# Performance work log

Hardware: AMD Instinct MI355X
Metric: run time of the kernel (lower is better)

## Reference

```python
import jax, jax.numpy as jnp
import numpy as np

INPUT_DIM = 2048
NUM_EXPERTS = 64
TOP_K = 2


def setup_inputs() -> dict:
    key = jax.random.key(0)
    kx, kw = jax.random.split(key)
    x = jax.random.normal(kx, (4, 4096, INPUT_DIM), dtype=jnp.float32)
    # nn.Linear weight has shape [num_experts, input_dim]
    W = jax.random.normal(kw, (NUM_EXPERTS, INPUT_DIM), dtype=jnp.float32) * (INPUT_DIM ** -0.5)
    return {"x": x, "W": W}


def reference(x, W):
    # Flatten tokens: [N, D]
    x_flat = x.reshape(-1, INPUT_DIM)
    # Gate logits: [N, E]
    gate_logits = jnp.einsum("nd,ed->ne", x_flat, W)
    # Top-k (sorted descending, matching torch.topk)
    top_k_logits, top_k_indices = jax.lax.top_k(gate_logits, TOP_K)
    top_k_values = jax.nn.softmax(top_k_logits, axis=-1)
    return (top_k_indices, top_k_values)
```

## Files before the change

kernel.cpp:

```cpp
#include <hip/hip_runtime.h>
#include <math.h>

typedef float f4 __attribute__((ext_vector_type(4)));
typedef float f32x4 __attribute__((ext_vector_type(4)));
typedef short bf16x8 __attribute__((ext_vector_type(8)));

#define D      2048
#define NE     64
#define TOKB   32
#define KSPLIT 4
#define KRNG   (D / KSPLIT)
#define KCH    32
#define NCH    (KRNG / KCH)
#define LROW   40
#define SLAB   10240

__device__ __forceinline__ unsigned short bf16rne(float f) {
    unsigned int u = __builtin_bit_cast(unsigned int, f);
    u += 0x7fffu + ((u >> 16) & 1u);
    return (unsigned short)(u >> 16);
}
__device__ __forceinline__ float bf2f(unsigned short h) {
    unsigned int u = (unsigned int)h << 16;
    return __builtin_bit_cast(float, u);
}

__global__ __launch_bounds__(256)
void wprep(const float* __restrict__ W,
           unsigned short* __restrict__ Wh,
           unsigned short* __restrict__ Wl)
{
    const int i = blockIdx.x * 256 + threadIdx.x;
    const float w = W[i];
    const unsigned short h = bf16rne(w);
    Wh[i] = h;
    Wl[i] = bf16rne(w - bf2f(h));
}

__global__ __launch_bounds__(256)
void moe_fused(const float* __restrict__ x,
               const unsigned short* __restrict__ Wh,
               const unsigned short* __restrict__ Wl,
               float* __restrict__ out, int ntok)
{
    __shared__ __align__(16) char smem[KSPLIT][SLAB];

    const int t    = threadIdx.x;
    const int w    = t >> 6;
    const int l    = t & 63;
    const int tok0 = blockIdx.x * TOKB;
    const int k0   = w * KRNG;

    unsigned short* stg = (unsigned short*)smem[w];

    const int srow = l >> 3;
    const int sg   = l & 7;
    const int ar   = l & 15;
    const int akb  = (l >> 4) * 8;
    const int be   = l & 15;

    const float* xbase = x + (size_t)tok0 * D + k0 + sg * 4;

    f4 xr0, xr1, xr2, xr3;

#define LOADX(ch) { \
    const float* p_ = xbase + (ch) * KCH; \
    xr0 = *(const f4*)(p_ + (size_t)(srow     ) * D); \
    xr1 = *(const f4*)(p_ + (size_t)(srow +  8) * D); \
    xr2 = *(const f4*)(p_ + (size_t)(srow + 16) * D); \
    xr3 = *(const f4*)(p_ + (size_t)(srow + 24) * D); }

#define CVT1(v, buf, row) { \
    unsigned short h0_=bf16rne(v.x), h1_=bf16rne(v.y), h2_=bf16rne(v.z), h3_=bf16rne(v.w); \
    unsigned short l0_=bf16rne(v.x-bf2f(h0_)), l1_=bf16rne(v.y-bf2f(h1_)); \
    unsigned short l2_=bf16rne(v.z-bf2f(h2_)), l3_=bf16rne(v.w-bf2f(h3_)); \
    uint2 hw_, lw_; \
    hw_.x=(unsigned)h0_|((unsigned)h1_<<16); hw_.y=(unsigned)h2_|((unsigned)h3_<<16); \
    lw_.x=(unsigned)l0_|((unsigned)l1_<<16); lw_.y=(unsigned)l2_|((unsigned)l3_<<16); \
    *(uint2*)&stg[(((buf)*2 + 0)*TOKB + (row))*LROW + sg*4] = hw_; \
    *(uint2*)&stg[(((buf)*2 + 1)*TOKB + (row))*LROW + sg*4] = lw_; }

#define CVTWR(buf) { CVT1(xr0, buf, srow); CVT1(xr1, buf, srow+8); \
                     CVT1(xr2, buf, srow+16); CVT1(xr3, buf, srow+24); }

    const f32x4 zz = {0.f, 0.f, 0.f, 0.f};
    f32x4 acc[2][4];
#pragma unroll
    for (int i = 0; i < 2; ++i)
#pragma unroll
        for (int j = 0; j < 4; ++j) acc[i][j] = zz;

    LOADX(0);
    CVTWR(0);

    for (int ch = 0; ch < NCH; ++ch) {
        bf16x8 bh[4], bl[4];
        const size_t kk = (size_t)(k0 + ch * KCH + akb);
#pragma unroll
        for (int et = 0; et < 4; ++et) {
            const size_t off = (size_t)(et * 16 + be) * D + kk;
            bh[et] = *(const bf16x8*)(Wh + off);
            bl[et] = *(const bf16x8*)(Wl + off);
        }
        if (ch + 1 < NCH) LOADX(ch + 1);

        bf16x8 ah[2], al[2];
        const int buf = ch & 1;
#pragma unroll
        for (int rt = 0; rt < 2; ++rt) {
            const int row = rt * 16 + ar;
            ah[rt] = *(const bf16x8*)&stg[((buf*2 + 0)*TOKB + row)*LROW + akb];
            al[rt] = *(const bf16x8*)&stg[((buf*2 + 1)*TOKB + row)*LROW + akb];
        }

#pragma unroll
        for (int rt = 0; rt < 2; ++rt)
#pragma unroll
            for (int et = 0; et < 4; ++et) {
                acc[rt][et] = __builtin_amdgcn_mfma_f32_16x16x32_bf16(ah[rt], bh[et], acc[rt][et], 0, 0, 0);
                acc[rt][et] = __builtin_amdgcn_mfma_f32_16x16x32_bf16(ah[rt], bl[et], acc[rt][et], 0, 0, 0);
                acc[rt][et] = __builtin_amdgcn_mfma_f32_16x16x32_bf16(al[rt], bh[et], acc[rt][et], 0, 0, 0);
            }

        if (ch + 1 < NCH) CVTWR((ch + 1) & 1);
    }

#undef LOADX
#undef CVT1
#undef CVTWR

    float* cred = (float*)smem[w];
#pragma unroll
    for (int rt = 0; rt < 2; ++rt)
#pragma unroll
        for (int et = 0; et < 4; ++et)
#pragma unroll
            for (int r = 0; r < 4; ++r) {
                const int tokl = rt * 16 + (l >> 4) * 4 + r;
                cred[tokl * 68 + et * 16 + (l & 15)] = acc[rt][et][r];
            }
    __syncthreads();

    {
        const int tokl = t >> 3;
        const int eg   = t & 7;
        f4 s0 = {0.f,0.f,0.f,0.f}, s1 = {0.f,0.f,0.f,0.f};
#pragma unroll
        for (int ww = 0; ww < 4; ++ww) {
            const float* cw = (const float*)smem[ww] + tokl * 68 + eg * 8;
            s0 += *(const f4*)cw;
            s1 += *(const f4*)(cw + 4);
        }
        const float vv[8] = {s0.x, s0.y, s0.z, s0.w, s1.x, s1.y, s1.z, s1.w};
        float m1 = -INFINITY, m2 = -INFINITY;
        int i1 = 0, i2 = 0;
#pragma unroll
        for (int j = 0; j < 8; ++j) {
            const float v = vv[j];
            const int id = eg * 8 + j;
            if (v > m1)      { m2 = m1; i2 = i1; m1 = v; i1 = id; }
            else if (v > m2) { m2 = v;  i2 = id; }
        }
#pragma unroll
        for (int m = 1; m < 8; m <<= 1) {
            const float om1 = __shfl_xor(m1, m);
            const int   oi1 = __shfl_xor(i1, m);
            const float om2 = __shfl_xor(m2, m);
            const int   oi2 = __shfl_xor(i2, m);
            const bool b1 = (om1 > m1) || (om1 == m1 && oi1 < i1);
            const float c2v = b1 ? m1 : om1;  const int c2i = b1 ? i1 : oi1;
            const float c3v = b1 ? om2 : m2;  const int c3i = b1 ? oi2 : i2;
            if (b1) { m1 = om1; i1 = oi1; }
            const bool b2 = (c3v > c2v) || (c3v == c2v && c3i < c2i);
            m2 = b2 ? c3v : c2v;  i2 = b2 ? c3i : c2i;
        }
        if (eg == 0) {
            const int tok = tok0 + tokl;
            out[(size_t)tok * 2 + 0] = (float)i1;
            out[(size_t)tok * 2 + 1] = (float)i2;
            const float p1 = 1.0f / (1.0f + expf(m2 - m1));
            float* vals = out + (size_t)ntok * 2;
            vals[(size_t)tok * 2 + 0] = p1;
            vals[(size_t)tok * 2 + 1] = 1.0f - p1;
        }
    }
}

extern "C" void kernel_launch(void* const* d_in, const int* in_sizes, int n_in,
                              void* d_out, int out_size, void* d_ws, size_t ws_size,
                              hipStream_t stream)
{
    const float* x = (const float*)d_in[0];
    const float* W = (const float*)d_in[1];
    float* out = (float*)d_out;
    unsigned short* Wh = (unsigned short*)d_ws;
    unsigned short* Wl = Wh + (size_t)NE * D;

    const int ntok = in_sizes[0] / D;
    wprep<<<(NE * D) / 256, 256, 0, stream>>>(W, Wh, Wl);
    moe_fused<<<ntok / TOKB, 256, 0, stream>>>(x, Wh, Wl, out, ntok);
}
```

Baseline: 46.28 us.

## Load x directly into MFMA operand registers, halve token tile, drop LDS staging

Halves the token block from 32 to 16 so each lane loads its own x row fragment straight from global memory in MFMA A-operand layout. This removes the LDS staging buffer and its store/load round trip. The split into hi/lo bf16 now uses packed bf16x2 conversion intrinsics, and the loop is unrolled by two with register double-buffering of x loads two chunks ahead. The trade-off is twice as many blocks, with W fragments reloaded per 16 tokens instead of per 32, which doubles W read traffic, and less MFMA work per W load.

```diff
diff --git a/kernel.cpp b/kernel.cpp
--- a/kernel.cpp
+++ b/kernel.cpp
@@ -1,19 +1,20 @@
 #include <hip/hip_runtime.h>
+#include <hip/hip_bf16.h>
 #include <math.h>
 
 typedef float f4 __attribute__((ext_vector_type(4)));
 typedef float f32x4 __attribute__((ext_vector_type(4)));
 typedef short bf16x8 __attribute__((ext_vector_type(8)));
+typedef unsigned int u32x4 __attribute__((ext_vector_type(4)));
 
 #define D      2048
 #define NE     64
-#define TOKB   32
+#define TOKB   16
 #define KSPLIT 4
 #define KRNG   (D / KSPLIT)
 #define KCH    32
 #define NCH    (KRNG / KCH)
-#define LROW   40
-#define SLAB   10240
+#define CSTR   68
 
 __device__ __forceinline__ unsigned short bf16rne(float f) {
     unsigned int u = __builtin_bit_cast(unsigned int, f);
@@ -37,13 +38,25 @@
     Wl[i] = bf16rne(w - bf2f(h));
 }
 
+#define CVTPAIR(F0, F1, HOUT, LOUT) {                                        \
+    __hip_bfloat162 hp_ = __float22bfloat162_rn(make_float2((F0), (F1)));    \
+    unsigned hu_; __builtin_memcpy(&hu_, &hp_, 4);                           \
+    const float h0_ = __builtin_bit_cast(float, hu_ << 16);                  \
+    const float h1_ = __builtin_bit_cast(float, hu_ & 0xffff0000u);          \
+    __hip_bfloat162 lp_ = __float22bfloat162_rn(                             \
+        make_float2((F0) - h0_, (F1) - h1_));                                \
+    unsigned lu_; __builtin_memcpy(&lu_, &lp_, 4);                           \
+    HOUT = hu_;                                                              \
+    LOUT = lu_;                                                              \
+}
+
 __global__ __launch_bounds__(256)
 void moe_fused(const float* __restrict__ x,
                const unsigned short* __restrict__ Wh,
                const unsigned short* __restrict__ Wl,
                float* __restrict__ out, int ntok)
 {
-    __shared__ __align__(16) char smem[KSPLIT][SLAB];
+    __shared__ float cred[KSPLIT][TOKB * CSTR];
 
     const int t    = threadIdx.x;
     const int w    = t >> 6;
@@ -51,103 +64,76 @@
     const int tok0 = blockIdx.x * TOKB;
     const int k0   = w * KRNG;
 
-    unsigned short* stg = (unsigned short*)smem[w];
+    const int ar  = l & 15;
+    const int akb = (l >> 4) * 8;
 
-    const int srow = l >> 3;
-    const int sg   = l & 7;
-    const int ar   = l & 15;
-    const int akb  = (l >> 4) * 8;
-    const int be   = l & 15;
-
-    const float* xbase = x + (size_t)tok0 * D + k0 + sg * 4;
-
-    f4 xr0, xr1, xr2, xr3;
-
-#define LOADX(ch) { \
-    const float* p_ = xbase + (ch) * KCH; \
-    xr0 = *(const f4*)(p_ + (size_t)(srow     ) * D); \
-    xr1 = *(const f4*)(p_ + (size_t)(srow +  8) * D); \
-    xr2 = *(const f4*)(p_ + (size_t)(srow + 16) * D); \
-    xr3 = *(const f4*)(p_ + (size_t)(srow + 24) * D); }
-
-#define CVT1(v, buf, row) { \
-    unsigned short h0_=bf16rne(v.x), h1_=bf16rne(v.y), h2_=bf16rne(v.z), h3_=bf16rne(v.w); \
-    unsigned short l0_=bf16rne(v.x-bf2f(h0_)), l1_=bf16rne(v.y-bf2f(h1_)); \
-    unsigned short l2_=bf16rne(v.z-bf2f(h2_)), l3_=bf16rne(v.w-bf2f(h3_)); \
-    uint2 hw_, lw_; \
-    hw_.x=(unsigned)h0_|((unsigned)h1_<<16); hw_.y=(unsigned)h2_|((unsigned)h3_<<16); \
-    lw_.x=(unsigned)l0_|((unsigned)l1_<<16); lw_.y=(unsigned)l2_|((unsigned)l3_<<16); \
-    *(uint2*)&stg[(((buf)*2 + 0)*TOKB + (row))*LROW + sg*4] = hw_; \
-    *(uint2*)&stg[(((buf)*2 + 1)*TOKB + (row))*LROW + sg*4] = lw_; }
-
-#define CVTWR(buf) { CVT1(xr0, buf, srow); CVT1(xr1, buf, srow+8); \
-                     CVT1(xr2, buf, srow+16); CVT1(xr3, buf, srow+24); }
+    const float*          xa  = x  + (size_t)(tok0 + ar) * D + k0 + akb;
+    const unsigned short* whb = Wh + (size_t)ar * D + k0 + akb;
+    const unsigned short* wlb = Wl + (size_t)ar * D + k0 + akb;
 
     const f32x4 zz = {0.f, 0.f, 0.f, 0.f};
-    f32x4 acc[2][4];
-#pragma unroll
-    for (int i = 0; i < 2; ++i)
-#pragma unroll
-        for (int j = 0; j < 4; ++j) acc[i][j] = zz;
+    f32x4 acc[4] = {zz, zz, zz, zz};
 
-    LOADX(0);
-    CVTWR(0);
+    f4 rA0 = *(const f4*)(xa);
+    f4 rA1 = *(const f4*)(xa + 4);
+    f4 rB0 = *(const f4*)(xa + KCH);
+    f4 rB1 = *(const f4*)(xa + KCH + 4);
 
-    for (int ch = 0; ch < NCH; ++ch) {
-        bf16x8 bh[4], bl[4];
-        const size_t kk = (size_t)(k0 + ch * KCH + akb);
-#pragma unroll
-        for (int et = 0; et < 4; ++et) {
-            const size_t off = (size_t)(et * 16 + be) * D + kk;
-            bh[et] = *(const bf16x8*)(Wh + off);
-            bl[et] = *(const bf16x8*)(Wl + off);
-        }
-        if (ch + 1 < NCH) LOADX(ch + 1);
+#define BODY(RA0, RA1, ch) {                                                 \
+             \
+    bf16x8 bh[4], bl[4];                                                     \
+    const size_t kk_ = (size_t)(ch) * KCH;                                   \
+    _Pragma("unroll")                                                        \
+    for (int et = 0; et < 4; ++et) {                                         \
+        bh[et] = *(const bf16x8*)(whb + (size_t)et * 16 * D + kk_);          \
+        bl[et] = *(const bf16x8*)(wlb + (size_t)et * 16 * D + kk_);          \
+    }                                                                        \
+                   \
+    unsigned hu0_, hu1_, hu2_, hu3_, lu0_, lu1_, lu2_, lu3_;                 \
+    CVTPAIR(RA0.x, RA0.y, hu0_, lu0_);                                       \
+    CVTPAIR(RA0.z, RA0.w, hu1_, lu1_);                                       \
+    CVTPAIR(RA1.x, RA1.y, hu2_, lu2_);                                       \
+    CVTPAIR(RA1.z, RA1.w, hu3_, lu3_);                                       \
+    const u32x4 hv_ = {hu0_, hu1_, hu2_, hu3_};                              \
+    const u32x4 lv_ = {lu0_, lu1_, lu2_, lu3_};                              \
+    const bf16x8 ah = __builtin_bit_cast(bf16x8, hv_);                       \
+    const bf16x8 al = __builtin_bit_cast(bf16x8, lv_);                       \
+           \
+    if ((ch) + 2 < NCH) {                                                    \
+        RA0 = *(const f4*)(xa + ((ch) + 2) * KCH);                           \
+        RA1 = *(const f4*)(xa + ((ch) + 2) * KCH + 4);                       \
+    }                                                                        \
+                            \
+    _Pragma("unroll")                                                        \
+    for (int et = 0; et < 4; ++et) {                                         \
+        acc[et] = __builtin_amdgcn_mfma_f32_16x16x32_bf16(ah, bh[et], acc[et], 0, 0, 0); \
+        acc[et] = __builtin_amdgcn_mfma_f32_16x16x32_bf16(ah, bl[et], acc[et], 0, 0, 0); \
+        acc[et] = __builtin_amdgcn_mfma_f32_16x16x32_bf16(al, bh[et], acc[et], 0, 0, 0); \
+    }                                                                        \
+}
 
-        bf16x8 ah[2], al[2];
-        const int buf = ch & 1;
-#pragma unroll
-        for (int rt = 0; rt < 2; ++rt) {
-            const int row = rt * 16 + ar;
-            ah[rt] = *(const bf16x8*)&stg[((buf*2 + 0)*TOKB + row)*LROW + akb];
-            al[rt] = *(const bf16x8*)&stg[((buf*2 + 1)*TOKB + row)*LROW + akb];
-        }
+    for (int ch = 0; ch < NCH; ch += 2) {
+        BODY(rA0, rA1, ch);
+        BODY(rB0, rB1, ch + 1);
+    }
+#undef BODY
 
 #pragma unroll
-        for (int rt = 0; rt < 2; ++rt)
+    for (int et = 0; et < 4; ++et)
 #pragma unroll
-            for (int et = 0; et < 4; ++et) {
-                acc[rt][et] = __builtin_amdgcn_mfma_f32_16x16x32_bf16(ah[rt], bh[et], acc[rt][et], 0, 0, 0);
-                acc[rt][et] = __builtin_amdgcn_mfma_f32_16x16x32_bf16(ah[rt], bl[et], acc[rt][et], 0, 0, 0);
-                acc[rt][et] = __builtin_amdgcn_mfma_f32_16x16x32_bf16(al[rt], bh[et], acc[rt][et], 0, 0, 0);
-            }
-
-        if (ch + 1 < NCH) CVTWR((ch + 1) & 1);
-    }
-
-#undef LOADX
-#undef CVT1
-#undef CVTWR
-
-    float* cred = (float*)smem[w];
-#pragma unroll
-    for (int rt = 0; rt < 2; ++rt)
-#pragma unroll
-        for (int et = 0; et < 4; ++et)
-#pragma unroll
-            for (int r = 0; r < 4; ++r) {
-                const int tokl = rt * 16 + (l >> 4) * 4 + r;
-                cred[tokl * 68 + et * 16 + (l & 15)] = acc[rt][et][r];
-            }
+        for (int r = 0; r < 4; ++r) {
+            const int tokl = (l >> 4) * 4 + r;
+            cred[w][tokl * CSTR + et * 16 + (l & 15)] = acc[et][r];
+        }
     __syncthreads();
 
-    {
+    if (t < TOKB * 8) {
         const int tokl = t >> 3;
         const int eg   = t & 7;
         f4 s0 = {0.f,0.f,0.f,0.f}, s1 = {0.f,0.f,0.f,0.f};
 #pragma unroll
-        for (int ww = 0; ww < 4; ++ww) {
-            const float* cw = (const float*)smem[ww] + tokl * 68 + eg * 8;
+        for (int ww = 0; ww < KSPLIT; ++ww) {
+            const float* cw = &cred[ww][tokl * CSTR + eg * 8];
             s0 += *(const f4*)cw;
             s1 += *(const f4*)(cw + 4);
         }
```

Measured after the change: 83.11 us. +79.6%, slower.
